# Kernel optimization log

Hardware: AMD Instinct MI355X
Metric: run time of the kernel (lower is better)

## Reference

```python
import jax, jax.numpy as jnp
import numpy as np

NUM_METAPATHS = 3
ETYPES = np.array([[0, 1], [2, 3], [4, 5]])  # [P, L-1], indices into expanded r_vec
N_NODES = 100000
N_TARGETS = 8192
E = 250000
L = 3
IN_DIM = 64
NUM_HEADS = 8
ATTN_VEC_DIM = 128
OUT_DIM = 64
ALPHA = 0.01  # LeakyReLU slope


def setup_inputs() -> dict:
    key = jax.random.key(0)
    ks = jax.random.split(key, 10)
    features = jax.random.normal(ks[0], (N_NODES, IN_DIM), jnp.float32)
    indices = jax.random.randint(ks[1], (NUM_METAPATHS, E, L), 0, N_NODES)
    dst = jax.random.randint(ks[2], (NUM_METAPATHS, E), 0, N_TARGETS)
    r_vec = jax.random.normal(ks[3], (3, IN_DIM // 2, 2), jnp.float32) * 0.5
    attn = jax.random.normal(ks[4], (NUM_METAPATHS, NUM_HEADS, IN_DIM), jnp.float32) * 0.1
    fc1_w = jax.random.normal(ks[5], (ATTN_VEC_DIM, IN_DIM * NUM_HEADS), jnp.float32) * 0.05
    fc1_b = jnp.zeros((ATTN_VEC_DIM,), jnp.float32)
    fc2_w = jax.random.normal(ks[6], (1, ATTN_VEC_DIM), jnp.float32) * 0.1
    fc_w = jax.random.normal(ks[7], (OUT_DIM, IN_DIM * NUM_HEADS), jnp.float32) * 0.05
    fc_b = jnp.zeros((OUT_DIM,), jnp.float32)
    return dict(features=features, indices=indices, dst=dst, r_vec=r_vec, attn=attn,
                fc1_w=fc1_w, fc1_b=fc1_b, fc2_w=fc2_w, fc_w=fc_w, fc_b=fc_b)


def _cmul(a, b):
    # complex multiply on trailing [..., 2] (real, imag) pairs
    re = a[..., 0] * b[..., 0] - a[..., 1] * b[..., 1]
    im = a[..., 0] * b[..., 1] + a[..., 1] * b[..., 0]
    return jnp.stack([re, im], axis=-1)


def _final_r_vec(r_full):
    # r_full: [num_edge_type, d2, 2] -> cumulative rotations per metapath [P, L, d2, 2]
    d2 = r_full.shape[1]
    one = jnp.stack([jnp.ones((d2,), r_full.dtype), jnp.zeros((d2,), r_full.dtype)], axis=-1)
    finals = []
    for p in range(NUM_METAPATHS):
        f = [None] * L
        f[L - 1] = one
        for i in range(L - 2, -1, -1):
            f[i] = _cmul(f[i + 1], r_full[int(ETYPES[p, i])])
        finals.append(jnp.stack(f))
    return jnp.stack(finals)  # [P, L, d2, 2]


def _forward(features, indices, dst, r_vec, attn, fc1_w, fc1_b, fc2_w, fc_w, fc_b):
    d2 = IN_DIM // 2
    # RotatE0: L2-normalize each complex rotation, then expand with conjugates
    r = r_vec / jnp.sqrt(jnp.sum(r_vec * r_vec, axis=-1, keepdims=True))
    r_conj = r * jnp.array([1.0, -1.0], r.dtype)
    r_full = jnp.stack([r, r_conj], axis=1).reshape(-1, d2, 2)  # [num_edge_type, d2, 2]
    final_r = _final_r_vec(r_full)  # [P, L, d2, 2]; final[L-1] = 1+0j (identity)

    def per_metapath(idx, d_idx, final_rv, attn_p):
        # idx: [E, L] node ids, d_idx: [E] destination (target) ids
        edata = features[idx].reshape(E, L, d2, 2)           # gather metapath instances
        edata = _cmul(edata, final_rv[None])                 # rotate each position
        hidden = edata.reshape(E, L, IN_DIM).mean(axis=1)    # [E, d]
        eft = jnp.broadcast_to(hidden[:, None, :], (E, NUM_HEADS, IN_DIM))
        a = jnp.einsum('ehd,hd->eh', eft, attn_p)
        a = jnp.where(a > 0, a, ALPHA * a)                   # leaky_relu
        # edge softmax per destination segment (stable)
        a_max = jax.ops.segment_max(a, d_idx, num_segments=N_TARGETS)
        a = jnp.exp(a - a_max[d_idx])
        a_sum = jax.ops.segment_sum(a, d_idx, num_segments=N_TARGETS)
        a = a / a_sum[d_idx]
        ft = jax.ops.segment_sum(eft * a[:, :, None], d_idx, num_segments=N_TARGETS)
        return ft.reshape(N_TARGETS, NUM_HEADS * IN_DIM)

    outs = jax.vmap(per_metapath)(indices, dst, final_r, attn)  # [P, Nt, H*d]
    outs = jax.nn.elu(outs)
    # inter-metapath attention
    fc1 = jnp.tanh(jnp.einsum('pnd,ad->pna', outs, fc1_w) + fc1_b)  # [P, Nt, A]
    beta = fc1.mean(axis=1) @ fc2_w.T                               # [P, 1]
    beta = jax.nn.softmax(beta[:, 0])                               # [P]
    h = jnp.einsum('p,pnd->nd', beta, outs)                         # [Nt, H*d]
    h_fc = h @ fc_w.T + fc_b                                        # [Nt, out_dim]
    return h_fc, h


def reference(features, indices, dst, r_vec, attn, fc1_w, fc1_b, fc2_w, fc_w, fc_b):
    return _forward(features, indices, dst, r_vec, attn, fc1_w, fc1_b, fc2_w, fc_w, fc_b)
```

## Files before the change

kernel.cpp:

```cpp
#include <hip/hip_runtime.h>
#include <hip/hip_bf16.h>
#include <hip/hip_fp16.h>

#define NP   3
#define NE   250000
#define NL   3
#define NT   8192
#define NN   100000
#define IND  64
#define ND2  32
#define NH   8
#define NAD  128
#define NOD  64
#define NHD  512
#define LALPHA 0.01f
#define NSEG (NP*NT)
#define NB   16

typedef __attribute__((ext_vector_type(8))) _Float16 half8;
typedef __attribute__((ext_vector_type(4))) _Float16 half4;
typedef __attribute__((ext_vector_type(4))) float f32x4;

#define FLAG_W    0
#define FINALR_W  64
#define ATILDE_W  704
#define BETAACC_N 5376
#define BETA_N    5760
#define COUNTS_N  6144
#define OFFS_N    30720
#define CURSOR_N  55360
#define EIDX_N    80000
#define ATTNF_N   3080000
#define FC1W_N    3081600
#define FC1B_N    3147136
#define FC2W_N    3147264
#define FCW_N     3147392
#define FCB_N     3180160
#define RVEC_N    3180224
#define FEATH_N   3180544
#define SCORE_N   6380544
#define OUTS_N    13580544
#define NEED_WORDS 19872000UL

#define BETAACC_F 1024
#define BETA_F    1472
#define COUNTS_F  2048
#define OFFS_F    26624
#define CURSOR_F  51264
#define ELIST_F   75904
#define FEATF_F   825920
#define ATTNF_F   7225920
#define FC1W_F    7227456
#define FC1B_F    7292992
#define FC2W_F    7293120
#define FCW_F     7293248
#define FCB_F     7326016
#define RVEC_F    7326080
#define OUTS_F    7326272

__device__ __forceinline__ float bf2f(unsigned short u) {
    union { unsigned int i; float f; } c; c.i = ((unsigned int)u) << 16; return c.f;
}

__global__ __launch_bounds__(256) void k_prep(
        const unsigned short* __restrict__ feat_raw,
        const void* __restrict__ rvec_src, const void* __restrict__ attn_src,
        const void* __restrict__ fc1b_src, const void* __restrict__ fc2w_src,
        const void* __restrict__ fcb_src,
        float* __restrict__ ws, int* __restrict__ flag,
        float* __restrict__ rvecf, float* __restrict__ attnf,
        float* __restrict__ fc1bf, float* __restrict__ fc2wf,
        float* __restrict__ fcbf) {
    __shared__ int cnt;
    int t = threadIdx.x;
    if (t == 0) cnt = 0;
    __syncthreads();
    int wild = 0;
    for (int i = t; i < 512; i += 256) {
        unsigned short u = feat_raw[i];
        int e = (u >> 7) & 0xFF;
        if (u != 0 && (e < 0x60 || e > 0x90)) wild++;
    }
    for (int off = 32; off; off >>= 1) wild += __shfl_xor(wild, off);
    if ((t & 63) == 0) atomicAdd(&cnt, wild);
    __syncthreads();
    int f = cnt > 64 ? 1 : 0;
    if (t == 0) *flag = f;
    for (int i = t; i < 192; i += 256)
        rvecf[i] = f ? ((const float*)rvec_src)[i] : bf2f(((const unsigned short*)rvec_src)[i]);
    for (int i = t; i < 1536; i += 256)
        attnf[i] = f ? ((const float*)attn_src)[i] : bf2f(((const unsigned short*)attn_src)[i]);
    if (t < 128) fc1bf[t] = f ? ((const float*)fc1b_src)[t] : bf2f(((const unsigned short*)fc1b_src)[t]);
    if (t < 128) fc2wf[t] = f ? ((const float*)fc2w_src)[t] : bf2f(((const unsigned short*)fc2w_src)[t]);
    if (t < 64)  fcbf[t]  = f ? ((const float*)fcb_src)[t]  : bf2f(((const unsigned short*)fcb_src)[t]);
    __syncthreads();
    if (t < NP * ND2) {
        int p = t / ND2, j = t % ND2;
        float re = rvecf[(p * ND2 + j) * 2 + 0];
        float im = rvecf[(p * ND2 + j) * 2 + 1];
        float inv = rsqrtf(re * re + im * im);
        float nre = re * inv, nim = im * inv;
        float f1r = nre, f1i = -nim;
        float f0r = f1r * nre - f1i * nim;
        float f0i = f1r * nim + f1i * nre;
        float* fr = ws + FINALR_W + p * NL * ND2 * 2;
        fr[(0 * ND2 + j) * 2 + 0] = f0r; fr[(0 * ND2 + j) * 2 + 1] = f0i;
        fr[(1 * ND2 + j) * 2 + 0] = f1r; fr[(1 * ND2 + j) * 2 + 1] = f1i;
        fr[(2 * ND2 + j) * 2 + 0] = 1.f; fr[(2 * ND2 + j) * 2 + 1] = 0.f;
    }
    __syncthreads();
    const float* finalr = ws + FINALR_W;
    float* atil = ws + ATILDE_W;
    for (int i = t; i < NP * NL * NH * IND; i += 256) {
        int d = i & 63, h = (i >> 6) & 7, l = (i >> 9) % 3, p = i / (64 * 8 * 3);
        int j = d >> 1; bool im = (d & 1) != 0;
        float cr = finalr[(p * NL * ND2 + l * ND2 + j) * 2 + 0];
        float ci = finalr[(p * NL * ND2 + l * ND2 + j) * 2 + 1];
        float ar = attnf[(p * NH + h) * IND + 2 * j];
        float ai = attnf[(p * NH + h) * IND + 2 * j + 1];
        float v = im ? (ai * cr - ar * ci) : (ar * cr + ai * ci);
        atil[i] = v * (1.f / 3.f);
    }
}

__global__ void k_cvt(const void* __restrict__ src, float* __restrict__ dst, int n,
                      const int* __restrict__ flag) {
    int i = blockIdx.x * blockDim.x + threadIdx.x;
    if (i >= n) return;
    if (*flag) dst[i] = ((const float*)src)[i];
    else       dst[i] = bf2f(((const unsigned short*)src)[i]);
}

__global__ void k_cvt_h4(const void* __restrict__ src, half4* __restrict__ dst, int n4,
                         const int* __restrict__ flag) {
    int i = blockIdx.x * blockDim.x + threadIdx.x;
    if (i >= n4) return;
    half4 o;
    if (*flag) {
        float4 v = ((const float4*)src)[i];
        o[0] = (_Float16)v.x; o[1] = (_Float16)v.y; o[2] = (_Float16)v.z; o[3] = (_Float16)v.w;
    } else {
        ushort4 u = ((const ushort4*)src)[i];
        o[0] = (_Float16)bf2f(u.x); o[1] = (_Float16)bf2f(u.y);
        o[2] = (_Float16)bf2f(u.z); o[3] = (_Float16)bf2f(u.w);
    }
    dst[i] = o;
}

__global__ void k_cvt_tr(const void* __restrict__ src, float* __restrict__ dst,
                         int R, int C, const int* __restrict__ flag) {
    int i = blockIdx.x * blockDim.x + threadIdx.x;
    if (i >= R * C) return;
    int r = i / C, c = i % C;
    float v;
    if (*flag) v = ((const float*)src)[i];
    else       v = bf2f(((const unsigned short*)src)[i]);
    dst[c * R + r] = v;
}

__global__ __launch_bounds__(256) void k_score(const void* __restrict__ feat_src,
                                               const int* __restrict__ flag,
                                               const float* __restrict__ atil,
                                               float* __restrict__ S,
                                               _Float16* __restrict__ featH) {
    __shared__ float xs[128][68];
    __shared__ float as[72][68];
    int t = threadIdx.x;
    int nbase = blockIdx.x * 128;
    int f = *flag;
    for (int i = t; i < 72 * 64; i += 256) as[i >> 6][i & 63] = atil[i];
    for (int c = t; c < 2048; c += 256) {
        int nloc = c >> 4, cc = c & 15;
        int node = nbase + nloc;
        float4 v;
        if (node < NN) {
            if (f) v = ((const float4*)feat_src)[(size_t)node * 16 + cc];
            else {
                ushort4 u = ((const ushort4*)feat_src)[(size_t)node * 16 + cc];
                v = make_float4(bf2f(u.x), bf2f(u.y), bf2f(u.z), bf2f(u.w));
            }
        } else v = make_float4(0.f, 0.f, 0.f, 0.f);
        int d0 = cc * 4;
        xs[nloc][d0 + 0] = v.x; xs[nloc][d0 + 1] = v.y;
        xs[nloc][d0 + 2] = v.z; xs[nloc][d0 + 3] = v.w;
        if (node < NN) {
            half4 hv;
            hv[0] = (_Float16)v.x; hv[1] = (_Float16)v.y;
            hv[2] = (_Float16)v.z; hv[3] = (_Float16)v.w;
            *(half4*)(featH + (size_t)node * IND + d0) = hv;
        }
    }
    __syncthreads();
    int lane = t & 63, w = t >> 6;
    int g = lane >> 3, h = lane & 7;
    int nloc = (w * 8 + g) * 4;
    float acc[9][4];
#pragma unroll
    for (int c = 0; c < 9; c++)
#pragma unroll
        for (int u = 0; u < 4; u++) acc[c][u] = 0.f;
    for (int ch = 0; ch < 16; ch++) {
        float4 xv[4];
#pragma unroll
        for (int u = 0; u < 4; u++) xv[u] = *(const float4*)&xs[nloc + u][ch * 4];
#pragma unroll
        for (int c = 0; c < 9; c++) {
            float4 av = *(const float4*)&as[c * 8 + h][ch * 4];
#pragma unroll
            for (int u = 0; u < 4; u++)
                acc[c][u] += xv[u].x * av.x + xv[u].y * av.y + xv[u].z * av.z + xv[u].w * av.w;
        }
    }
#pragma unroll
    for (int u = 0; u < 4; u++) {
        int node = nbase + nloc + u;
        if (node < NN) {
#pragma unroll
            for (int c = 0; c < 9; c++)
                S[(long)node * 72 + c * 8 + h] = acc[c][u];
        }
    }
}

__global__ void k_count(const int* __restrict__ dst, int* __restrict__ counts) {
    int id = blockIdx.x * blockDim.x + threadIdx.x;
    if (id >= NP * NE) return;
    int p = id / NE;
    atomicAdd(&counts[p * NT + dst[id]], 1);
}

__global__ __launch_bounds__(256) void k_scan(const int* __restrict__ counts,
                                              int* __restrict__ offs,
                                              int* __restrict__ cursor) {
    __shared__ int wtot[4];
    int t = threadIdx.x;
    const int CH = NSEG / 256;
    int base = t * CH;
    int s = 0;
    for (int i = 0; i < CH; i++) s += counts[base + i];
    int l = t & 63, w = t >> 6;
    int v = s;
    for (int off = 1; off < 64; off <<= 1) {
        int u = __shfl_up(v, off);
        if (l >= off) v += u;
    }
    if (l == 63) wtot[w] = v;
    __syncthreads();
    int wb = 0;
    for (int i = 0; i < w; i++) wb += wtot[i];
    int run = wb + v - s;
    for (int i = 0; i < CH; i++) {
        int c = counts[base + i];
        offs[base + i] = run; cursor[base + i] = run;
        run += c;
    }
    if (t == 255) offs[NSEG] = wb + v;
}

__global__ void k_scatter2(const int* __restrict__ dst, const int* __restrict__ indices,
                           int* __restrict__ cursor, int4* __restrict__ eidx) {
    int id = blockIdx.x * blockDim.x + threadIdx.x;
    if (id >= NP * NE) return;
    int p = id / NE, e = id % NE;
    int pos = atomicAdd(&cursor[p * NT + dst[id]], 1);
    const int* ip = indices + (long)p * NE * NL + (long)e * NL;
    eidx[pos] = make_int4(ip[0], ip[1], ip[2], 0);
}

__global__ void k_scatter(const int* __restrict__ dst, int* __restrict__ cursor,
                          int* __restrict__ elist) {
    int id = blockIdx.x * blockDim.x + threadIdx.x;
    if (id >= NP * NE) return;
    int p = id / NE, e = id % NE;
    int pos = atomicAdd(&cursor[p * NT + dst[id]], 1);
    elist[pos] = e;
}

__global__ __launch_bounds__(64) void k_agg2(
        const _Float16* __restrict__ featH, const int4* __restrict__ eidx,
        const float* __restrict__ S, const float* __restrict__ finalr,
        const int* __restrict__ offs, _Float16* __restrict__ outs) {
    int b = blockIdx.x;
    int p = b / NT;
    int t = threadIdx.x;
    int h = t >> 3, q = t & 7;

    const unsigned sB = (unsigned)((p * 24 + h) * 4);
    const unsigned fB = (unsigned)(q << 4);
    const char* Sb = (const char*)S;
    const char* Fb = (const char*)featH;

    float a0[8], a1[8], a2[8];
#pragma unroll
    for (int r = 0; r < 8; r++) { a0[r] = 0.f; a1[r] = 0.f; a2[r] = 0.f; }
    float se = 0.f;

    int beg = offs[b], end = offs[b + 1];

    int i = beg;
    for (; i + 4 <= end; i += 4) {
        int4 ee[4];
        float s0v[4], s1v[4], s2v[4];
        half8 x0[4], x1[4], x2[4];
#pragma unroll
        for (int u = 0; u < 4; u++) ee[u] = eidx[i + u];
#pragma unroll
        for (int u = 0; u < 4; u++) {
            unsigned ox = (unsigned)ee[u].x, oy = (unsigned)ee[u].y, oz = (unsigned)ee[u].z;
            s0v[u] = *(const float*)(Sb + (ox * 288u + sB));
            s1v[u] = *(const float*)(Sb + (oy * 288u + sB) + 32);
            s2v[u] = *(const float*)(Sb + (oz * 288u + sB) + 64);
            x0[u] = *(const half8*)(Fb + ((ox << 7) + fB));
            x1[u] = *(const half8*)(Fb + ((oy << 7) + fB));
            x2[u] = *(const half8*)(Fb + ((oz << 7) + fB));
        }
#pragma unroll
        for (int u = 0; u < 4; u++) {
            float s = s0v[u] + s1v[u] + s2v[u];
            float a = s > 0.f ? s : LALPHA * s;
            float eh = __expf(a);
            se += eh;
#pragma unroll
            for (int r = 0; r < 8; r++) {
                a0[r] += eh * (float)x0[u][r];
                a1[r] += eh * (float)x1[u][r];
                a2[r] += eh * (float)x2[u][r];
            }
        }
    }
    for (; i < end; i++) {
        int4 e = eidx[i];
        unsigned ox = (unsigned)e.x, oy = (unsigned)e.y, oz = (unsigned)e.z;
        float s = *(const float*)(Sb + (ox * 288u + sB))
                + *(const float*)(Sb + (oy * 288u + sB) + 32)
                + *(const float*)(Sb + (oz * 288u + sB) + 64);
        float a = s > 0.f ? s : LALPHA * s;
        float eh = __expf(a);
        se += eh;
        half8 x0 = *(const half8*)(Fb + ((ox << 7) + fB));
        half8 x1 = *(const half8*)(Fb + ((oy << 7) + fB));
        half8 x2 = *(const half8*)(Fb + ((oz << 7) + fB));
#pragma unroll
        for (int r = 0; r < 8; r++) {
            a0[r] += eh * (float)x0[r];
            a1[r] += eh * (float)x1[r];
            a2[r] += eh * (float)x2[r];
        }
    }

    const float* fr = finalr + p * NL * ND2 * 2;
    float sc = (end > beg) ? (1.f / 3.f) / se : 0.f;
    half8 o;
#pragma unroll
    for (int jj = 0; jj < 4; jj++) {
        int j = 4 * q + jj;
        float c0r = fr[(0 * ND2 + j) * 2 + 0], c0i = fr[(0 * ND2 + j) * 2 + 1];
        float c1r = fr[(1 * ND2 + j) * 2 + 0], c1i = fr[(1 * ND2 + j) * 2 + 1];
        float ar, ai, vr, vi;
        ar = a0[2 * jj]; ai = a0[2 * jj + 1];
        vr = ar * c0r - ai * c0i; vi = ar * c0i + ai * c0r;
        ar = a1[2 * jj]; ai = a1[2 * jj + 1];
        vr += ar * c1r - ai * c1i; vi += ar * c1i + ai * c1r;
        vr += a2[2 * jj]; vi += a2[2 * jj + 1];
        vr *= sc; vi *= sc;
        vr = vr > 0.f ? vr : __expf(vr) - 1.f;
        vi = vi > 0.f ? vi : __expf(vi) - 1.f;
        o[2 * jj]     = (_Float16)vr;
        o[2 * jj + 1] = (_Float16)vi;
    }
    *(half8*)(outs + (long)b * NHD + (h << 6) + (q << 3)) = o;
}

__global__ __launch_bounds__(64) void k_agg(
        const float* __restrict__ feat, const int* __restrict__ indices,
        const float* __restrict__ attn, const float* __restrict__ ws_f,
        const int* __restrict__ offs, const int* __restrict__ elist,
        _Float16* __restrict__ outs) {
    int b = blockIdx.x;
    int p = b / NT;
    int d = threadIdx.x;
    int j = d >> 1;
    bool isim = (d & 1) != 0;
    const float* fr = ws_f + FINALR_W + p * NL * ND2 * 2;
    float cr[NL], ci[NL];
#pragma unroll
    for (int l = 0; l < NL; l++) {
        cr[l] = fr[(l * ND2 + j) * 2 + 0];
        ci[l] = fr[(l * ND2 + j) * 2 + 1];
    }
    float at[NH];
#pragma unroll
    for (int h = 0; h < NH; h++) at[h] = attn[(p * NH + h) * IND + d];
    float ft[NH], se[NH];
#pragma unroll
    for (int h = 0; h < NH; h++) { ft[h] = 0.f; se[h] = 0.f; }
    int beg = offs[b], end = offs[b + 1];
    const int* idxp = indices + (long)p * NE * NL;
    for (int i = beg; i < end; i++) {
        int e = elist[i];
        int nn[3] = { idxp[e * 3 + 0], idxp[e * 3 + 1], idxp[e * 3 + 2] };
        float hid = 0.f;
#pragma unroll
        for (int l = 0; l < NL; l++) {
            float x = feat[(long)nn[l] * IND + d];
            float xp = __shfl_xor(x, 1);
            float re = isim ? xp : x;
            float im = isim ? x : xp;
            hid += isim ? (re * ci[l] + im * cr[l]) : (re * cr[l] - im * ci[l]);
        }
        hid *= (1.f / 3.f);
#pragma unroll
        for (int h = 0; h < NH; h++) {
            float v = hid * at[h];
#pragma unroll
            for (int off = 32; off; off >>= 1) v += __shfl_xor(v, off);
            float a = v > 0.f ? v : LALPHA * v;
            float eh = __expf(a);
            se[h] += eh;
            ft[h] += eh * hid;
        }
    }
    _Float16* orow = outs + (long)b * NHD;
    bool has = end > beg;
#pragma unroll
    for (int h = 0; h < NH; h++) {
        float v = has ? ft[h] / fmaxf(se[h], 1e-20f) : 0.f;
        v = v > 0.f ? v : (__expf(v) - 1.f);
        orow[h * IND + d] = (_Float16)v;
    }
}

__global__ __launch_bounds__(256) void k_fc1(
        const _Float16* __restrict__ outs, const _Float16* __restrict__ fc1h,
        const float* __restrict__ fc1_b, float* __restrict__ betaacc) {
    __shared__ float red[4][NAD];
    int tid = threadIdx.x;
    int wid = tid >> 6, lane = tid & 63;
    int nt = blockIdx.x * 4 + wid;
    int p  = blockIdx.x / (NT / 16 / 4);
    int col = lane & 15, kq = lane >> 4;

    const _Float16* brow  = outs + ((long)nt * 16 + col) * NHD + kq * 8;
    const _Float16* abase = fc1h + (long)col * NHD + kq * 8;

    f32x4 acc[8];
#pragma unroll
    for (int ta = 0; ta < 8; ta++) acc[ta] = (f32x4){0.f, 0.f, 0.f, 0.f};

    for (int kk = 0; kk < 16; kk++) {
        half8 b = *(const half8*)(brow + kk * 32);
#pragma unroll
        for (int ta = 0; ta < 8; ta++) {
            half8 a = *(const half8*)(abase + (long)ta * 16 * NHD + kk * 32);
            acc[ta] = __builtin_amdgcn_mfma_f32_16x16x32_f16(a, b, acc[ta], 0, 0, 0);
        }
    }

#pragma unroll
    for (int ta = 0; ta < 8; ta++) {
#pragma unroll
        for (int r = 0; r < 4; r++) {
            int arow = ta * 16 + kq * 4 + r;
            float v = tanhf(acc[ta][r] + fc1_b[arow]);
            v += __shfl_xor(v, 1); v += __shfl_xor(v, 2);
            v += __shfl_xor(v, 4); v += __shfl_xor(v, 8);
            if (col == 0) red[wid][arow] = v;
        }
    }
    __syncthreads();
    if (tid < NAD) {
        float s = red[0][tid] + red[1][tid] + red[2][tid] + red[3][tid];
        atomicAdd(&betaacc[p * NAD + tid], s);
    }
}

__global__ void k_beta(const float* __restrict__ betaacc,
                       const float* __restrict__ fc2_w, float* __restrict__ beta) {
    __shared__ float lds[NP][NAD];
    int t = threadIdx.x;
    for (int p = 0; p < NP; p++)
        lds[p][t] = betaacc[p * NAD + t] * (1.f / NT) * fc2_w[t];
    __syncthreads();
    if (t == 0) {
        float s[NP];
        for (int p = 0; p < NP; p++) {
            s[p] = 0.f;
            for (int a = 0; a < NAD; a++) s[p] += lds[p][a];
        }
        float m = fmaxf(s[0], fmaxf(s[1], s[2]));
        float e0 = expf(s[0] - m), e1 = expf(s[1] - m), e2 = expf(s[2] - m);
        float inv = 1.f / (e0 + e1 + e2);
        beta[0] = e0 * inv; beta[1] = e1 * inv; beta[2] = e2 * inv;
    }
}

__global__ __launch_bounds__(256) void k_final(
        const _Float16* __restrict__ outs, const float* __restrict__ beta,
        const float* __restrict__ fc_wT, const float* __restrict__ fc_b,
        void* __restrict__ outp, const int* __restrict__ flag) {
    __shared__ float h[NB * NHD];
    __shared__ float part[4 * NB * NOD];
    int n0 = blockIdx.x * NB;
    int t = threadIdx.x;
    int f = *flag;
    float b0 = beta[0], b1 = beta[1], b2 = beta[2];
    const _Float16* o0 = outs + (long)n0 * NHD;
    for (int i = t; i < NB * NHD / 8; i += 256) {
        half8 v0 = *(const half8*)(o0 + i * 8);
        half8 v1 = *(const half8*)(o0 + (long)NT * NHD + i * 8);
        half8 v2 = *(const half8*)(o0 + 2L * NT * NHD + i * 8);
#pragma unroll
        for (int jj = 0; jj < 8; jj++) {
            float v = b0 * (float)v0[jj] + b1 * (float)v1[jj] + b2 * (float)v2[jj];
            h[i * 8 + jj] = v;
            long idx = (long)NT * NOD + (long)n0 * NHD + i * 8 + jj;
            if (f) ((float*)outp)[idx] = v;
            else   ((__hip_bfloat16*)outp)[idx] = __float2bfloat16(v);
        }
    }
    __syncthreads();
    int w = t >> 6, l = t & 63;
    float acc[NB];
#pragma unroll
    for (int n = 0; n < NB; n++) acc[n] = 0.f;
    for (int k = w * 128; k < (w + 1) * 128; k++) {
        float wv = fc_wT[k * NOD + l];
#pragma unroll
        for (int n = 0; n < NB; n++) acc[n] += h[n * NHD + k] * wv;
    }
#pragma unroll
    for (int n = 0; n < NB; n++) part[(w * NB + n) * NOD + l] = acc[n];
    __syncthreads();
    for (int idx = t; idx < NB * NOD; idx += 256) {
        int n = idx >> 6, ll = idx & 63;
        float v = part[(0 * NB + n) * NOD + ll] + part[(1 * NB + n) * NOD + ll]
                + part[(2 * NB + n) * NOD + ll] + part[(3 * NB + n) * NOD + ll]
                + fc_b[ll];
        long oidx = (long)(n0 + n) * NOD + ll;
        if (f) ((float*)outp)[oidx] = v;
        else   ((__hip_bfloat16*)outp)[oidx] = __float2bfloat16(v);
    }
}

extern "C" void kernel_launch(void* const* d_in, const int* in_sizes, int n_in,
                              void* d_out, int out_size, void* d_ws, size_t ws_size,
                              hipStream_t stream) {
    const int* indices = (const int*)d_in[1];
    const int* dst     = (const int*)d_in[2];

    float* ws  = (float*)d_ws;
    int*   wsi = (int*)d_ws;

    bool big = ws_size >= NEED_WORDS * 4UL;

    const int betaacc = big ? BETAACC_N : BETAACC_F;
    const int beta    = big ? BETA_N    : BETA_F;
    const int counts  = big ? COUNTS_N  : COUNTS_F;
    const int offs    = big ? OFFS_N    : OFFS_F;
    const int cursor  = big ? CURSOR_N  : CURSOR_F;
    const int attnf   = big ? ATTNF_N   : ATTNF_F;
    const int fc1w    = big ? FC1W_N    : FC1W_F;
    const int fc1b    = big ? FC1B_N    : FC1B_F;
    const int fc2w    = big ? FC2W_N    : FC2W_F;
    const int fcw     = big ? FCW_N     : FCW_F;
    const int fcb     = big ? FCB_N     : FCB_F;
    const int rvec    = big ? RVEC_N    : RVEC_F;
    const int outsw   = big ? OUTS_N    : OUTS_F;
    _Float16* outsp = (_Float16*)(ws + outsw);
    _Float16* fc1h  = (_Float16*)(ws + fc1w);

    hipMemsetAsync((char*)d_ws + (size_t)counts * 4, 0, NSEG * 4, stream);
    hipMemsetAsync((char*)d_ws + (size_t)betaacc * 4, 0, NP * NAD * 4, stream);

    k_prep<<<1, 256, 0, stream>>>((const unsigned short*)d_in[0],
                                  d_in[3], d_in[4], d_in[6], d_in[7], d_in[9],
                                  ws, wsi + FLAG_W,
                                  ws + rvec, ws + attnf, ws + fc1b, ws + fc2w,
                                  ws + fcb);

    k_cvt_h4<<<(NAD * NHD / 4 + 255) / 256, 256, 0, stream>>>(d_in[5], (half4*)fc1h,
                                                              NAD * NHD / 4, wsi + FLAG_W);
    k_cvt_tr<<<(NOD * NHD + 255) / 256, 256, 0, stream>>>(d_in[8], ws + fcw,
                                                          NOD, NHD, wsi + FLAG_W);
    k_count<<<(NP * NE + 255) / 256, 256, 0, stream>>>(dst, wsi + counts);
    k_scan<<<1, 256, 0, stream>>>(wsi + counts, wsi + offs, wsi + cursor);

    if (big) {
        _Float16* featH = (_Float16*)(ws + FEATH_N);
        k_score<<<(NN + 127) / 128, 256, 0, stream>>>(d_in[0], wsi + FLAG_W,
                                                      ws + ATILDE_W, ws + SCORE_N, featH);
        k_scatter2<<<(NP * NE + 255) / 256, 256, 0, stream>>>(dst, indices,
                                                              wsi + cursor,
                                                              (int4*)(wsi + EIDX_N));
        k_agg2<<<NSEG, 64, 0, stream>>>(featH, (const int4*)(wsi + EIDX_N),
                                        ws + SCORE_N, ws + FINALR_W,
                                        wsi + offs, outsp);
    } else {
        k_cvt<<<(NN * IND + 255) / 256, 256, 0, stream>>>(d_in[0], ws + FEATF_F,
                                                          NN * IND, wsi + FLAG_W);
        k_scatter<<<(NP * NE + 255) / 256, 256, 0, stream>>>(dst, wsi + cursor,
                                                             wsi + ELIST_F);
        k_agg<<<NSEG, 64, 0, stream>>>(ws + FEATF_F, indices, ws + attnf, ws,
                                       wsi + offs, wsi + ELIST_F, outsp);
    }

    k_fc1<<<NP * NT / 16 / 4, 256, 0, stream>>>(outsp, fc1h, ws + fc1b, ws + betaacc);
    k_beta<<<1, 128, 0, stream>>>(ws + betaacc, ws + fc2w, ws + beta);
    k_final<<<NT / NB, 256, 0, stream>>>(outsp, ws + beta, ws + fcw, ws + fcb,
                                         d_out, wsi + FLAG_W);
}
```

Measured before the change: 354.5 us.

## Precompute per-edge attention exponentials in a separate kernel before aggregation

Adds a k_escore kernel that computes, for every sorted edge and head, the summed node scores, LeakyReLU and exp, and writes them to a new workspace buffer. The aggregation kernel then reads one precomputed value per edge and head instead of three scattered score loads plus an exp. This is meant to cut the random gathers and latency inside the aggregation's critical loop. In exchange it adds a kernel launch and about 24 MB of extra global writes and reads, and the score gathers still happen, only in a different kernel.

```diff
diff --git a/kernel.cpp b/kernel.cpp
--- a/kernel.cpp
+++ b/kernel.cpp
@@ -40,7 +40,8 @@
 #define FEATH_N   3180544
 #define SCORE_N   6380544
 #define OUTS_N    13580544
-#define NEED_WORDS 19872000UL
+#define EH_N      19872000
+#define NEED_WORDS 25872000UL
 
 #define BETAACC_F 1024
 #define BETA_F    1472
@@ -276,49 +277,55 @@
     elist[pos] = e;
 }
 
+__global__ __launch_bounds__(256) void k_escore(const int4* __restrict__ eidx,
+                                                const float* __restrict__ S,
+                                                float* __restrict__ EH) {
+    int id = blockIdx.x * 256 + threadIdx.x;
+    if (id >= NP * NE * 8) return;
+    int pos = id >> 3, h = id & 7;
+    int p = pos / NE;
+    int4 e = eidx[pos];
+    const float* Sp = S + p * 24 + h;
+    float s = Sp[(long)e.x * 72] + Sp[(long)e.y * 72 + 8] + Sp[(long)e.z * 72 + 16];
+    float a = fmaxf(s, LALPHA * s);
+    EH[id] = __expf(a);
+}
+
 __global__ __launch_bounds__(64) void k_agg2(
         const _Float16* __restrict__ featH, const int4* __restrict__ eidx,
-        const float* __restrict__ S, const float* __restrict__ finalr,
+        const float* __restrict__ EH, const float* __restrict__ finalr,
         const int* __restrict__ offs, _Float16* __restrict__ outs) {
     int b = blockIdx.x;
     int p = b / NT;
     int t = threadIdx.x;
     int h = t >> 3, q = t & 7;
 
-    const unsigned sB = (unsigned)((p * 24 + h) * 4);
-    const unsigned fB = (unsigned)(q << 4);
-    const char* Sb = (const char*)S;
-    const char* Fb = (const char*)featH;
-
     float a0[8], a1[8], a2[8];
 #pragma unroll
     for (int r = 0; r < 8; r++) { a0[r] = 0.f; a1[r] = 0.f; a2[r] = 0.f; }
     float se = 0.f;
 
     int beg = offs[b], end = offs[b + 1];
+    const float* EHh = EH + h;
 
     int i = beg;
     for (; i + 4 <= end; i += 4) {
         int4 ee[4];
-        float s0v[4], s1v[4], s2v[4];
+        float ehv[4];
         half8 x0[4], x1[4], x2[4];
 #pragma unroll
+        for (int u = 0; u < 4; u++) ehv[u] = EHh[(long)(i + u) * 8];
+#pragma unroll
         for (int u = 0; u < 4; u++) ee[u] = eidx[i + u];
 #pragma unroll
         for (int u = 0; u < 4; u++) {
-            unsigned ox = (unsigned)ee[u].x, oy = (unsigned)ee[u].y, oz = (unsigned)ee[u].z;
-            s0v[u] = *(const float*)(Sb + (ox * 288u + sB));
-            s1v[u] = *(const float*)(Sb + (oy * 288u + sB) + 32);
-            s2v[u] = *(const float*)(Sb + (oz * 288u + sB) + 64);
-            x0[u] = *(const half8*)(Fb + ((ox << 7) + fB));
-            x1[u] = *(const half8*)(Fb + ((oy << 7) + fB));
-            x2[u] = *(const half8*)(Fb + ((oz << 7) + fB));
+            x0[u] = *(const half8*)(featH + ((long)ee[u].x << 6) + (q << 3));
+            x1[u] = *(const half8*)(featH + ((long)ee[u].y << 6) + (q << 3));
+            x2[u] = *(const half8*)(featH + ((long)ee[u].z << 6) + (q << 3));
         }
 #pragma unroll
         for (int u = 0; u < 4; u++) {
-            float s = s0v[u] + s1v[u] + s2v[u];
-            float a = s > 0.f ? s : LALPHA * s;
-            float eh = __expf(a);
+            float eh = ehv[u];
             se += eh;
 #pragma unroll
             for (int r = 0; r < 8; r++) {
@@ -330,16 +337,11 @@
     }
     for (; i < end; i++) {
         int4 e = eidx[i];
-        unsigned ox = (unsigned)e.x, oy = (unsigned)e.y, oz = (unsigned)e.z;
-        float s = *(const float*)(Sb + (ox * 288u + sB))
-                + *(const float*)(Sb + (oy * 288u + sB) + 32)
-                + *(const float*)(Sb + (oz * 288u + sB) + 64);
-        float a = s > 0.f ? s : LALPHA * s;
-        float eh = __expf(a);
+        float eh = EHh[(long)i * 8];
         se += eh;
-        half8 x0 = *(const half8*)(Fb + ((ox << 7) + fB));
-        half8 x1 = *(const half8*)(Fb + ((oy << 7) + fB));
-        half8 x2 = *(const half8*)(Fb + ((oz << 7) + fB));
+        half8 x0 = *(const half8*)(featH + ((long)e.x << 6) + (q << 3));
+        half8 x1 = *(const half8*)(featH + ((long)e.y << 6) + (q << 3));
+        half8 x2 = *(const half8*)(featH + ((long)e.z << 6) + (q << 3));
 #pragma unroll
         for (int r = 0; r < 8; r++) {
             a0[r] += eh * (float)x0[r];
@@ -592,8 +594,10 @@
         k_scatter2<<<(NP * NE + 255) / 256, 256, 0, stream>>>(dst, indices,
                                                               wsi + cursor,
                                                               (int4*)(wsi + EIDX_N));
+        k_escore<<<(NP * NE * 8 + 255) / 256, 256, 0, stream>>>(
+            (const int4*)(wsi + EIDX_N), ws + SCORE_N, ws + EH_N);
         k_agg2<<<NSEG, 64, 0, stream>>>(featH, (const int4*)(wsi + EIDX_N),
-                                        ws + SCORE_N, ws + FINALR_W,
+                                        ws + EH_N, ws + FINALR_W,
                                         wsi + offs, outsp);
     } else {
         k_cvt<<<(NN * IND + 255) / 256, 256, 0, stream>>>(d_in[0], ws + FEATF_F,
```

Result: no change. 360.8 us (+1.8%).
